# Performance work log

Hardware: AMD Instinct MI355X
Metric: run time of the kernel (lower is better)

The kernel has to match this reference:

```python
import jax, jax.numpy as jnp
import numpy as np

N = 50000   # nodes
E = 300000  # edges (before self-loops)
G = 64      # graphs in batch
F = 64      # feature_dim
H = 4       # n_head
C = 64      # per-head out channels (= feature_dim)
LAT = 256   # latent_dim
NEG_SLOPE = 0.2  # PyG GATConv default


def setup_inputs() -> dict:
    key = jax.random.key(0)
    ks = jax.random.split(key, 32)
    f32 = jnp.float32

    def w(k, shape, fan_in):
        return jax.random.normal(k, shape, dtype=f32) * (1.0 / np.sqrt(fan_in))

    return {
        "building_feature": jax.random.normal(ks[0], (N, 5), dtype=f32),
        "edge_index": jax.random.randint(ks[1], (2, E), 0, N, dtype=jnp.int32),
        "batch": jnp.sort(jax.random.randint(ks[2], (N,), 0, G, dtype=jnp.int32)),
        "bf_W": w(ks[3], (5, F), 5), "bf_b": jnp.zeros((F,), f32),
        "W1": w(ks[4], (F, H * C), F), "as1": w(ks[5], (H, C), C), "ad1": w(ks[6], (H, C), C), "b1": jnp.zeros((H * C,), f32),
        "W2": w(ks[7], (H * C, H * C), H * C), "as2": w(ks[8], (H, C), C), "ad2": w(ks[9], (H, C), C), "b2": jnp.zeros((H * C,), f32),
        "W3": w(ks[10], (H * C, H * C), H * C), "as3": w(ks[11], (H, C), C), "ad3": w(ks[12], (H, C), C), "b3": jnp.zeros((H * C,), f32),
        "agg_W": w(ks[13], (F * (1 + H * 3), LAT), F * (1 + H * 3)), "agg_b": jnp.zeros((LAT,), f32),
        "mu_W": w(ks[14], (LAT, LAT), LAT), "mu_b": jnp.zeros((LAT,), f32),
        "var_W": w(ks[15], (LAT, LAT), LAT), "var_b": jnp.zeros((LAT,), f32),
    }


def _gat_conv(x, W, att_src, att_dst, bias, src, dst):
    # PyG GATConv, concat=True, add_self_loops already in src/dst.
    h = (x @ W).reshape(-1, H, C)                       # [N,H,C]
    a_s = jnp.einsum("nhc,hc->nh", h, att_src)          # [N,H]
    a_d = jnp.einsum("nhc,hc->nh", h, att_dst)
    e = jax.nn.leaky_relu(a_s[src] + a_d[dst], NEG_SLOPE)  # [E,H]
    # segment softmax over incoming edges of each dst node
    m = jax.ops.segment_max(e, dst, num_segments=N)
    p = jnp.exp(e - m[dst])
    s = jax.ops.segment_sum(p, dst, num_segments=N)
    alpha = p / s[dst]                                  # [E,H]
    out = jax.ops.segment_sum(alpha[:, :, None] * h[src], dst, num_segments=N)
    return out.reshape(-1, H * C) + bias


def reference(building_feature, edge_index, batch,
              bf_W, bf_b,
              W1, as1, ad1, b1,
              W2, as2, ad2, b2,
              W3, as3, ad3, b3,
              agg_W, agg_b, mu_W, mu_b, var_W, var_b):
    # add self-loops (PyG GATConv default add_self_loops=True)
    loops = jnp.arange(N, dtype=edge_index.dtype)
    src = jnp.concatenate([edge_index[0], loops])
    dst = jnp.concatenate([edge_index[1], loops])

    n0 = jax.nn.relu(building_feature @ bf_W + bf_b)                 # [N,F]
    n1 = jax.nn.relu(_gat_conv(n0, W1, as1, ad1, b1, src, dst))      # [N,H*C]
    n2 = jax.nn.relu(_gat_conv(n1, W2, as2, ad2, b2, src, dst))
    n3 = jax.nn.relu(_gat_conv(n2, W3, as3, ad3, b3, src, dst))

    g = jnp.concatenate([
        jax.ops.segment_max(n0, batch, num_segments=G),
        jax.ops.segment_max(n1, batch, num_segments=G),
        jax.ops.segment_max(n2, batch, num_segments=G),
        jax.ops.segment_max(n3, batch, num_segments=G),
    ], axis=1)                                                       # [G, F*(1+3H)]

    latent = g @ agg_W + agg_b
    mu = latent @ mu_W + mu_b
    log_var = latent @ var_W + var_b
    return mu, log_var
```

## Files before the change

### kernel.cpp

```cpp
#include <hip/hip_runtime.h>
#include <hip/hip_bf16.h>

#define NN 50000
#define NPAD 50048
#define EE 300000
#define ETOT (EE + NN)
#define GG 64
#define GCOLS 832
#define LATD 256
#define BM 128
#define BN 128
#define NB_SCAN 196
#define LOG2E 1.4426950408889634f

typedef unsigned short u16;
typedef short s16x8 __attribute__((ext_vector_type(8)));
typedef float f32x4 __attribute__((ext_vector_type(4)));

__device__ __forceinline__ u16 f2bf(float f) {
    union { float f; unsigned u; } v; v.f = f;
    unsigned r = v.u + 0x7FFFu + ((v.u >> 16) & 1u);
    return (u16)(r >> 16);
}
__device__ __forceinline__ float bf2f(u16 u) {
    union { unsigned u; float f; } v; v.u = ((unsigned)u) << 16;
    return v.f;
}

__global__ __launch_bounds__(256) void k_prep(const float* __restrict__ W1, const float* __restrict__ W2,
                                              const float* __restrict__ W3, u16* __restrict__ Wt1,
                                              u16* __restrict__ Wt2, u16* __restrict__ Wt3,
                                              const float* __restrict__ bf, const float* __restrict__ Wb,
                                              const float* __restrict__ bb, const int* __restrict__ batch,
                                              u16* __restrict__ n0bf, int* __restrict__ gbuf,
                                              const int* __restrict__ ei, int* __restrict__ counts,
                                              u16* __restrict__ nbf) {
    int b = blockIdx.x;
    if (b < 576) {
        int idx = b * 256 + threadIdx.x;
        if (idx < 16384) {
            int n = idx >> 6, k = idx & 63;
            Wt1[idx] = f2bf(W1[k * 256 + n]);
        } else if (idx < 81920) {
            int t = idx - 16384; int n = t >> 8, k = t & 255;
            Wt2[t] = f2bf(W2[k * 256 + n]);
        } else {
            int t = idx - 81920; int n = t >> 8, k = t & 255;
            Wt3[t] = f2bf(W3[k * 256 + n]);
        }
    } else if (b < 967) {
        int c = threadIdx.x & 63;
        int sub = threadIdx.x >> 6;
        int base = (b - 576) * 128;
        int end = min(base + 128, NN);
        float w0 = Wb[c], w1 = Wb[64 + c], w2 = Wb[128 + c], w3 = Wb[192 + c], w4 = Wb[256 + c], bb_ = bb[c];
        float mx = 0.f;
        int curg = -1;
        for (int n = base + sub; n < end; n += 4) {
            const float* r = bf + (size_t)n * 5;
            float v = bb_ + r[0] * w0 + r[1] * w1 + r[2] * w2 + r[3] * w3 + r[4] * w4;
            v = fmaxf(v, 0.f);
            n0bf[(size_t)n * 64 + c] = f2bf(v);
            int g = batch[n];
            if (g != curg) {
                if (curg >= 0) atomicMax(&gbuf[curg * GCOLS + c], __float_as_int(mx));
                mx = 0.f; curg = g;
            }
            mx = fmaxf(mx, v);
        }
        if (curg >= 0) atomicMax(&gbuf[curg * GCOLS + c], __float_as_int(mx));
    } else if (b < 2335) {
        int e = (b - 967) * 256 + threadIdx.x;
        if (e < ETOT) {
            int d = (e < EE) ? ei[EE + e] : (e - EE);
            atomicAdd(&counts[d], 1);
        }
    } else {
        u16* p0 = n0bf + (size_t)NN * 64;
        for (int i = threadIdx.x; i < (NPAD - NN) * 64; i += 256) p0[i] = 0;
        u16* p1 = nbf + (size_t)NN * 256;
        for (int i = threadIdx.x; i < (NPAD - NN) * 256; i += 256) p1[i] = 0;
    }
}

__global__ __launch_bounds__(256) void k_scan_block(const int* __restrict__ counts, int* __restrict__ scanned,
                                                    int* __restrict__ bsums, int n) {
    __shared__ int sh[256];
    int i = blockIdx.x * 256 + threadIdx.x;
    int v = (i < n) ? counts[i] : 0;
    sh[threadIdx.x] = v; __syncthreads();
    for (int d = 1; d < 256; d <<= 1) {
        int t = (threadIdx.x >= d) ? sh[threadIdx.x - d] : 0;
        __syncthreads();
        sh[threadIdx.x] += t;
        __syncthreads();
    }
    if (i < n) scanned[i] = sh[threadIdx.x] - v;
    if (threadIdx.x == 255) bsums[blockIdx.x] = sh[255];
}

__global__ __launch_bounds__(256) void k_scan_add2(const int* __restrict__ scanned, const int* __restrict__ bsums,
                                                   int* __restrict__ indptr, int* __restrict__ fill) {
    __shared__ int sh[256];
    int t = threadIdx.x;
    int v = (t < NB_SCAN) ? bsums[t] : 0;
    sh[t] = v; __syncthreads();
    for (int d = 1; d < 256; d <<= 1) {
        int u = (t >= d) ? sh[t - d] : 0;
        __syncthreads();
        sh[t] += u;
        __syncthreads();
    }
    int bix = blockIdx.x;
    int boff = (bix == 0) ? 0 : sh[bix - 1];
    int i = bix * 256 + t;
    if (i < NN) { indptr[i] = scanned[i] + boff; fill[i] = 0; }
    if (i == 0) indptr[NN] = ETOT;
}

__global__ __launch_bounds__(256) void k_fill(const int* __restrict__ ei, const int* __restrict__ indptr,
                                              int* __restrict__ fill, int* __restrict__ esrc) {
    int e = blockIdx.x * 256 + threadIdx.x;
    if (e >= ETOT) return;
    int s, d;
    if (e < EE) { s = ei[e]; d = ei[EE + e]; } else { s = d = e - EE; }
    int pos = atomicAdd(&fill[d], 1);
    esrc[indptr[d] + pos] = s;
}

__global__ __launch_bounds__(256) void k_gemm_mfma(const u16* __restrict__ A,
                                                   const u16* __restrict__ Bt,
                                                   const float* __restrict__ att_s,
                                                   const float* __restrict__ att_d,
                                                   u16* __restrict__ Hbf,
                                                   float* __restrict__ a_s,
                                                   float* __restrict__ a_d,
                                                   int K) {
    __shared__ __align__(16) u16 As[128 * 64];
    __shared__ __align__(16) u16 Bs[128 * 64];
    const int tid = threadIdx.x;
    const int lane = tid & 63;
    const int w = tid >> 6;
    const int wr = w >> 1, wc = w & 1;
    const int row0 = blockIdx.x * BM;
    const int col0 = blockIdx.y * BN;

    f32x4 acc[4][4] = {};

    for (int kt = 0; kt < K; kt += 64) {
#pragma unroll
        for (int i = 0; i < 4; ++i) {
            int u = i * 256 + tid;
            int r = u >> 3, c16 = u & 7;
            int sc = ((c16 ^ (r & 7)) << 3);
            const u16* ga = A + (size_t)(row0 + r) * K + kt + sc;
            u16* la = &As[(size_t)(i * 256 + (w << 6)) * 8];
            __builtin_amdgcn_global_load_lds((const __attribute__((address_space(1))) void*)ga,
                                             (__attribute__((address_space(3))) void*)la, 16, 0, 0);
        }
#pragma unroll
        for (int i = 0; i < 4; ++i) {
            int u = i * 256 + tid;
            int r = u >> 3, c16 = u & 7;
            int sc = ((c16 ^ (r & 7)) << 3);
            const u16* gb = Bt + (size_t)(col0 + r) * K + kt + sc;
            u16* lb = &Bs[(size_t)(i * 256 + (w << 6)) * 8];
            __builtin_amdgcn_global_load_lds((const __attribute__((address_space(1))) void*)gb,
                                             (__attribute__((address_space(3))) void*)lb, 16, 0, 0);
        }
        __syncthreads();
#pragma unroll
        for (int ks = 0; ks < 2; ++ks) {
            s16x8 af[4], bfr[4];
#pragma unroll
            for (int m = 0; m < 4; ++m) {
                int ra = wr * 64 + m * 16 + (lane & 15);
                int c16 = ks * 4 + (lane >> 4);
                int off = ra * 64 + ((c16 ^ (ra & 7)) << 3);
                af[m] = *reinterpret_cast<const s16x8*>(&As[off]);
            }
#pragma unroll
            for (int n = 0; n < 4; ++n) {
                int rb = wc * 64 + n * 16 + (lane & 15);
                int c16 = ks * 4 + (lane >> 4);
                int off = rb * 64 + ((c16 ^ (rb & 7)) << 3);
                bfr[n] = *reinterpret_cast<const s16x8*>(&Bs[off]);
            }
#pragma unroll
            for (int m = 0; m < 4; ++m)
#pragma unroll
                for (int n = 0; n < 4; ++n)
                    acc[m][n] = __builtin_amdgcn_mfma_f32_16x16x32_bf16(af[m], bfr[n], acc[m][n], 0, 0, 0);
        }
        __syncthreads();
    }

    const int head = (blockIdx.y << 1) + wc;
    float asv[4], adv[4];
#pragma unroll
    for (int n = 0; n < 4; ++n) {
        asv[n] = att_s[head * 64 + n * 16 + (lane & 15)] * LOG2E;
        adv[n] = att_d[head * 64 + n * 16 + (lane & 15)] * LOG2E;
    }
#pragma unroll
    for (int m = 0; m < 4; ++m) {
        int growb = row0 + wr * 64 + m * 16 + (lane >> 4) * 4;
#pragma unroll
        for (int j = 0; j < 4; ++j) {
            int grow = growb + j;
            u16* orow = Hbf + (size_t)grow * 256 + col0 + wc * 64 + (lane & 15);
            float vs = 0.f, vd = 0.f;
#pragma unroll
            for (int n = 0; n < 4; ++n) {
                float v = acc[m][n][j];
                orow[n * 16] = f2bf(v);
                vs += v * asv[n];
                vd += v * adv[n];
            }
            vs += __shfl_xor(vs, 1); vd += __shfl_xor(vd, 1);
            vs += __shfl_xor(vs, 2); vd += __shfl_xor(vd, 2);
            vs += __shfl_xor(vs, 4); vd += __shfl_xor(vd, 4);
            vs += __shfl_xor(vs, 8); vd += __shfl_xor(vd, 8);
            if ((lane & 15) == 0) {
                a_s[grow * 4 + head] = vs;
                a_d[grow * 4 + head] = vd;
            }
        }
    }
}

__global__ __launch_bounds__(1024) void k_agg(const u16* __restrict__ Hbf, const float* __restrict__ a_s,
                                              const float* __restrict__ a_d, const int* __restrict__ indptr,
                                              const int* __restrict__ esrc, const float* __restrict__ bias,
                                              const int* __restrict__ batch, u16* __restrict__ outbf,
                                              int* __restrict__ gbuf, int poolOff) {
    __shared__ int lpool[2][256];
    if (threadIdx.x < 512) lpool[threadIdx.x >> 8][threadIdx.x & 255] = 0;
    __syncthreads();

    const int nodeBase = blockIdx.x * 16;
    const int wv = threadIdx.x >> 6;
    const int wid = nodeBase + wv;
    const int lane = threadIdx.x & 63;
    const int h = lane >> 4;
    const int eidx = lane & 15;
    const bool active = wid < NN;

    if (active) {
        int beg = indptr[wid];
        int dcount = indptr[wid + 1] - beg;
        float ad = a_d[wid * 4 + h];
        float mx = -3.0e38f, ssum = 0.f;
        float ax = 0.f, ay = 0.f, az = 0.f, aw = 0.f;

        for (int cb = 0; cb < dcount; cb += 16) {
            int cnt = min(16, dcount - cb);
            int s = (eidx < cnt) ? esrc[beg + cb + eidx] : 0;
            float el = (eidx < cnt) ? a_s[s * 4 + h] + ad : -3.0e38f;
            el = fmaxf(el, 0.2f * el);
            float cm = el;
            cm = fmaxf(cm, __shfl_xor(cm, 1));
            cm = fmaxf(cm, __shfl_xor(cm, 2));
            cm = fmaxf(cm, __shfl_xor(cm, 4));
            cm = fmaxf(cm, __shfl_xor(cm, 8));
            float nm = fmaxf(mx, cm);
            if (__any(nm > mx)) {
                float corr = exp2f(mx - nm);
                ssum *= corr; ax *= corr; ay *= corr; az *= corr; aw *= corr;
                mx = nm;
            }
            float p = exp2f(el - mx);
            float cs = p;
            cs += __shfl_xor(cs, 1);
            cs += __shfl_xor(cs, 2);
            cs += __shfl_xor(cs, 4);
            cs += __shfl_xor(cs, 8);
            ssum += cs;
            int e2 = 0;
            for (; e2 + 2 <= cnt; e2 += 2) {
                int s0 = __shfl(s, e2), s1 = __shfl(s, e2 + 1);
                float p0 = __shfl(p, (lane & 48) | e2);
                float p1 = __shfl(p, (lane & 48) | (e2 + 1));
                const ushort4 h0 = *reinterpret_cast<const ushort4*>(Hbf + (size_t)s0 * 256 + lane * 4);
                const ushort4 h1 = *reinterpret_cast<const ushort4*>(Hbf + (size_t)s1 * 256 + lane * 4);
                ax += p0 * bf2f(h0.x) + p1 * bf2f(h1.x);
                ay += p0 * bf2f(h0.y) + p1 * bf2f(h1.y);
                az += p0 * bf2f(h0.z) + p1 * bf2f(h1.z);
                aw += p0 * bf2f(h0.w) + p1 * bf2f(h1.w);
            }
            if (e2 < cnt) {
                int s0 = __shfl(s, e2);
                float p0 = __shfl(p, (lane & 48) | e2);
                const ushort4 h0 = *reinterpret_cast<const ushort4*>(Hbf + (size_t)s0 * 256 + lane * 4);
                ax += p0 * bf2f(h0.x);
                ay += p0 * bf2f(h0.y);
                az += p0 * bf2f(h0.z);
                aw += p0 * bf2f(h0.w);
            }
        }

        float inv = 1.0f / ssum;
        const float4 bv = *reinterpret_cast<const float4*>(bias + lane * 4);
        float o0 = fmaxf(ax * inv + bv.x, 0.f);
        float o1 = fmaxf(ay * inv + bv.y, 0.f);
        float o2 = fmaxf(az * inv + bv.z, 0.f);
        float o3 = fmaxf(aw * inv + bv.w, 0.f);
        ushort4 ob; ob.x = f2bf(o0); ob.y = f2bf(o1); ob.z = f2bf(o2); ob.w = f2bf(o3);
        *reinterpret_cast<ushort4*>(outbf + (size_t)wid * 256 + lane * 4) = ob;

        int g = batch[wid];
        int g0 = batch[nodeBase];
        int slot = g - g0;
        int c4 = lane * 4;
        if (slot < 2) {
            atomicMax(&lpool[slot][c4],     __float_as_int(o0));
            atomicMax(&lpool[slot][c4 + 1], __float_as_int(o1));
            atomicMax(&lpool[slot][c4 + 2], __float_as_int(o2));
            atomicMax(&lpool[slot][c4 + 3], __float_as_int(o3));
        } else {
            int* cell = &gbuf[g * GCOLS + poolOff + c4];
            atomicMax(cell,     __float_as_int(o0));
            atomicMax(cell + 1, __float_as_int(o1));
            atomicMax(cell + 2, __float_as_int(o2));
            atomicMax(cell + 3, __float_as_int(o3));
        }
    }
    __syncthreads();
    if (threadIdx.x < 512) {
        int slot = threadIdx.x >> 8, c = threadIdx.x & 255;
        int v = lpool[slot][c];
        if (v != 0) {
            int g0 = batch[nodeBase];
            atomicMax(&gbuf[(g0 + slot) * GCOLS + poolOff + c], v);
        }
    }
}

__global__ __launch_bounds__(256) void k_head(const int* __restrict__ gbuf,
                                              const float* __restrict__ aggW, const float* __restrict__ aggb,
                                              const float* __restrict__ muW, const float* __restrict__ mub,
                                              const float* __restrict__ varW, const float* __restrict__ varb,
                                              float* __restrict__ out) {
    __shared__ float lat[LATD];
    int gi = blockIdx.x, j = threadIdx.x;
    const float* g = (const float*)gbuf + (size_t)gi * GCOLS;
    float acc = aggb[j];
    for (int k = 0; k < GCOLS; ++k) acc += g[k] * aggW[k * 256 + j];
    lat[j] = acc;
    __syncthreads();
    float am = mub[j], av = varb[j];
    for (int k = 0; k < 256; ++k) {
        float l = lat[k];
        am += l * muW[k * 256 + j];
        av += l * varW[k * 256 + j];
    }
    out[(size_t)gi * 256 + j] = am;
    out[(size_t)GG * 256 + (size_t)gi * 256 + j] = av;
}

extern "C" void kernel_launch(void* const* d_in, const int* in_sizes, int n_in,
                              void* d_out, int out_size, void* d_ws, size_t ws_size,
                              hipStream_t stream) {
    const float* bf   = (const float*)d_in[0];
    const int*   ei   = (const int*)d_in[1];
    const int*   batch= (const int*)d_in[2];
    const float* bf_W = (const float*)d_in[3];
    const float* bf_b = (const float*)d_in[4];
    const float* W1   = (const float*)d_in[5];
    const float* as1  = (const float*)d_in[6];
    const float* ad1  = (const float*)d_in[7];
    const float* b1   = (const float*)d_in[8];
    const float* W2   = (const float*)d_in[9];
    const float* as2  = (const float*)d_in[10];
    const float* ad2  = (const float*)d_in[11];
    const float* b2   = (const float*)d_in[12];
    const float* W3   = (const float*)d_in[13];
    const float* as3  = (const float*)d_in[14];
    const float* ad3  = (const float*)d_in[15];
    const float* b3   = (const float*)d_in[16];
    const float* aggW = (const float*)d_in[17];
    const float* aggb = (const float*)d_in[18];
    const float* muW  = (const float*)d_in[19];
    const float* mub  = (const float*)d_in[20];
    const float* varW = (const float*)d_in[21];
    const float* varb = (const float*)d_in[22];
    float* out = (float*)d_out;

    size_t off = 0;
    auto alloc = [&](size_t bytes) -> char* {
        char* p = (char*)d_ws + off;
        off += (bytes + 255) & ~(size_t)255;
        return p;
    };
    int*   counts  = (int*)alloc((size_t)(NN + GG * GCOLS) * 4);
    int*   gbuf    = counts + NN;
    u16*   Hbf     = (u16*)alloc((size_t)NPAD * 256 * 2);
    u16*   n0bf    = (u16*)alloc((size_t)NPAD * 64 * 2);
    u16*   nbf     = (u16*)alloc((size_t)NPAD * 256 * 2);
    float* a_s     = (float*)alloc((size_t)NPAD * 4 * 4);
    float* a_d     = (float*)alloc((size_t)NPAD * 4 * 4);
    int*   scanned = (int*)alloc((size_t)NN * 4);
    int*   bsums   = (int*)alloc(256 * 4);
    int*   indptr  = (int*)alloc((size_t)(NN + 1) * 4);
    int*   fill    = (int*)alloc((size_t)NN * 4);
    int*   esrc    = (int*)alloc((size_t)ETOT * 4);
    u16*   Wt1     = (u16*)alloc((size_t)256 * 64 * 2);
    u16*   Wt2     = (u16*)alloc((size_t)256 * 256 * 2);
    u16*   Wt3     = (u16*)alloc((size_t)256 * 256 * 2);

    hipMemsetAsync(counts, 0, (size_t)(NN + GG * GCOLS) * 4, stream);

    k_prep<<<2336, 256, 0, stream>>>(W1, W2, W3, Wt1, Wt2, Wt3,
                                     bf, bf_W, bf_b, batch, n0bf, gbuf,
                                     ei, counts, nbf);

    k_scan_block<<<NB_SCAN, 256, 0, stream>>>(counts, scanned, bsums, NN);
    k_scan_add2<<<NB_SCAN, 256, 0, stream>>>(scanned, bsums, indptr, fill);
    k_fill<<<(ETOT + 255) / 256, 256, 0, stream>>>(ei, indptr, fill, esrc);

    dim3 ggrid(NPAD / BM, 256 / BN);
    const int AB = NN / 16;

    k_gemm_mfma<<<ggrid, 256, 0, stream>>>(n0bf, Wt1, as1, ad1, Hbf, a_s, a_d, 64);
    k_agg<<<AB, 1024, 0, stream>>>(Hbf, a_s, a_d, indptr, esrc, b1, batch, nbf, gbuf, 64);

    k_gemm_mfma<<<ggrid, 256, 0, stream>>>(nbf, Wt2, as2, ad2, Hbf, a_s, a_d, 256);
    k_agg<<<AB, 1024, 0, stream>>>(Hbf, a_s, a_d, indptr, esrc, b2, batch, nbf, gbuf, 320);

    k_gemm_mfma<<<ggrid, 256, 0, stream>>>(nbf, Wt3, as3, ad3, Hbf, a_s, a_d, 256);
    k_agg<<<AB, 1024, 0, stream>>>(Hbf, a_s, a_d, indptr, esrc, b3, batch, nbf, gbuf, 576);

    k_head<<<GG, 256, 0, stream>>>(gbuf, aggW, aggb, muW, mub, varW, varb, out);
}
```

Measured before the change: 275.9 us.

## Shrink aggregation blocks, unroll gather by four, restructure pooling and split head GEMV

The aggregation kernel now uses 8-node, 512-thread blocks with no bounds check, since 50000 divides evenly by 8. Its gather loop is unrolled to four edges per step so more loads are in flight. Per-block graph max-pooling now goes through a shared-memory reduction instead of shared atomics. The head kernel spreads each GEMV's K dimension across 1024 threads and reduces the partials in shared memory, which addresses the low parallelism of 64 blocks of 256 threads. The trade-offs are more aggregation blocks and more register pressure from the unroll.

```diff
diff --git a/kernel.cpp b/kernel.cpp
--- a/kernel.cpp
+++ b/kernel.cpp
@@ -229,133 +229,134 @@
     }
 }
 
-__global__ __launch_bounds__(1024) void k_agg(const u16* __restrict__ Hbf, const float* __restrict__ a_s,
-                                              const float* __restrict__ a_d, const int* __restrict__ indptr,
-                                              const int* __restrict__ esrc, const float* __restrict__ bias,
-                                              const int* __restrict__ batch, u16* __restrict__ outbf,
-                                              int* __restrict__ gbuf, int poolOff) {
-    __shared__ int lpool[2][256];
-    if (threadIdx.x < 512) lpool[threadIdx.x >> 8][threadIdx.x & 255] = 0;
-    __syncthreads();
-
-    const int nodeBase = blockIdx.x * 16;
+__global__ __launch_bounds__(512) void k_agg(const u16* __restrict__ Hbf, const float* __restrict__ a_s,
+                                             const float* __restrict__ a_d, const int* __restrict__ indptr,
+                                             const int* __restrict__ esrc, const float* __restrict__ bias,
+                                             const int* __restrict__ batch, u16* __restrict__ outbf,
+                                             int* __restrict__ gbuf, int poolOff) {
+    __shared__ float smax[8][256];
+    __shared__ int sb[8];
+    const int nodeBase = blockIdx.x * 8;
     const int wv = threadIdx.x >> 6;
     const int wid = nodeBase + wv;
     const int lane = threadIdx.x & 63;
     const int h = lane >> 4;
     const int eidx = lane & 15;
-    const bool active = wid < NN;
-
-    if (active) {
-        int beg = indptr[wid];
-        int dcount = indptr[wid + 1] - beg;
-        float ad = a_d[wid * 4 + h];
-        float mx = -3.0e38f, ssum = 0.f;
-        float ax = 0.f, ay = 0.f, az = 0.f, aw = 0.f;
-
-        for (int cb = 0; cb < dcount; cb += 16) {
-            int cnt = min(16, dcount - cb);
-            int s = (eidx < cnt) ? esrc[beg + cb + eidx] : 0;
-            float el = (eidx < cnt) ? a_s[s * 4 + h] + ad : -3.0e38f;
-            el = fmaxf(el, 0.2f * el);
-            float cm = el;
-            cm = fmaxf(cm, __shfl_xor(cm, 1));
-            cm = fmaxf(cm, __shfl_xor(cm, 2));
-            cm = fmaxf(cm, __shfl_xor(cm, 4));
-            cm = fmaxf(cm, __shfl_xor(cm, 8));
-            float nm = fmaxf(mx, cm);
-            if (__any(nm > mx)) {
-                float corr = exp2f(mx - nm);
-                ssum *= corr; ax *= corr; ay *= corr; az *= corr; aw *= corr;
-                mx = nm;
-            }
-            float p = exp2f(el - mx);
-            float cs = p;
-            cs += __shfl_xor(cs, 1);
-            cs += __shfl_xor(cs, 2);
-            cs += __shfl_xor(cs, 4);
-            cs += __shfl_xor(cs, 8);
-            ssum += cs;
-            int e2 = 0;
-            for (; e2 + 2 <= cnt; e2 += 2) {
-                int s0 = __shfl(s, e2), s1 = __shfl(s, e2 + 1);
-                float p0 = __shfl(p, (lane & 48) | e2);
-                float p1 = __shfl(p, (lane & 48) | (e2 + 1));
-                const ushort4 h0 = *reinterpret_cast<const ushort4*>(Hbf + (size_t)s0 * 256 + lane * 4);
-                const ushort4 h1 = *reinterpret_cast<const ushort4*>(Hbf + (size_t)s1 * 256 + lane * 4);
-                ax += p0 * bf2f(h0.x) + p1 * bf2f(h1.x);
-                ay += p0 * bf2f(h0.y) + p1 * bf2f(h1.y);
-                az += p0 * bf2f(h0.z) + p1 * bf2f(h1.z);
-                aw += p0 * bf2f(h0.w) + p1 * bf2f(h1.w);
-            }
-            if (e2 < cnt) {
-                int s0 = __shfl(s, e2);
-                float p0 = __shfl(p, (lane & 48) | e2);
-                const ushort4 h0 = *reinterpret_cast<const ushort4*>(Hbf + (size_t)s0 * 256 + lane * 4);
-                ax += p0 * bf2f(h0.x);
-                ay += p0 * bf2f(h0.y);
-                az += p0 * bf2f(h0.z);
-                aw += p0 * bf2f(h0.w);
-            }
-        }
-
-        float inv = 1.0f / ssum;
-        const float4 bv = *reinterpret_cast<const float4*>(bias + lane * 4);
-        float o0 = fmaxf(ax * inv + bv.x, 0.f);
-        float o1 = fmaxf(ay * inv + bv.y, 0.f);
-        float o2 = fmaxf(az * inv + bv.z, 0.f);
-        float o3 = fmaxf(aw * inv + bv.w, 0.f);
-        ushort4 ob; ob.x = f2bf(o0); ob.y = f2bf(o1); ob.z = f2bf(o2); ob.w = f2bf(o3);
-        *reinterpret_cast<ushort4*>(outbf + (size_t)wid * 256 + lane * 4) = ob;
-
-        int g = batch[wid];
-        int g0 = batch[nodeBase];
-        int slot = g - g0;
-        int c4 = lane * 4;
-        if (slot < 2) {
-            atomicMax(&lpool[slot][c4],     __float_as_int(o0));
-            atomicMax(&lpool[slot][c4 + 1], __float_as_int(o1));
-            atomicMax(&lpool[slot][c4 + 2], __float_as_int(o2));
-            atomicMax(&lpool[slot][c4 + 3], __float_as_int(o3));
-        } else {
-            int* cell = &gbuf[g * GCOLS + poolOff + c4];
-            atomicMax(cell,     __float_as_int(o0));
-            atomicMax(cell + 1, __float_as_int(o1));
-            atomicMax(cell + 2, __float_as_int(o2));
-            atomicMax(cell + 3, __float_as_int(o3));
-        }
-    }
+
+    if (threadIdx.x < 8) sb[threadIdx.x] = batch[nodeBase + threadIdx.x];
     __syncthreads();
-    if (threadIdx.x < 512) {
-        int slot = threadIdx.x >> 8, c = threadIdx.x & 255;
-        int v = lpool[slot][c];
-        if (v != 0) {
-            int g0 = batch[nodeBase];
-            atomicMax(&gbuf[(g0 + slot) * GCOLS + poolOff + c], v);
-        }
-    }
-}
-
-__global__ __launch_bounds__(256) void k_head(const int* __restrict__ gbuf,
-                                              const float* __restrict__ aggW, const float* __restrict__ aggb,
-                                              const float* __restrict__ muW, const float* __restrict__ mub,
-                                              const float* __restrict__ varW, const float* __restrict__ varb,
-                                              float* __restrict__ out) {
+
+    int beg = indptr[wid];
+    int dcount = indptr[wid + 1] - beg;
+    float ad = a_d[wid * 4 + h];
+    float mx = -3.0e38f, ssum = 0.f;
+    float ax = 0.f, ay = 0.f, az = 0.f, aw = 0.f;
+
+    for (int cb = 0; cb < dcount; cb += 16) {
+        int cnt = min(16, dcount - cb);
+        int s = (eidx < cnt) ? esrc[beg + cb + eidx] : 0;
+        float el = (eidx < cnt) ? a_s[s * 4 + h] + ad : -3.0e38f;
+        el = fmaxf(el, 0.2f * el);
+        float cm = el;
+        cm = fmaxf(cm, __shfl_xor(cm, 1));
+        cm = fmaxf(cm, __shfl_xor(cm, 2));
+        cm = fmaxf(cm, __shfl_xor(cm, 4));
+        cm = fmaxf(cm, __shfl_xor(cm, 8));
+        float nm = fmaxf(mx, cm);
+        if (__any(nm > mx)) {
+            float corr = exp2f(mx - nm);
+            ssum *= corr; ax *= corr; ay *= corr; az *= corr; aw *= corr;
+            mx = nm;
+        }
+        float p = exp2f(el - mx);
+        float cs = p;
+        cs += __shfl_xor(cs, 1);
+        cs += __shfl_xor(cs, 2);
+        cs += __shfl_xor(cs, 4);
+        cs += __shfl_xor(cs, 8);
+        ssum += cs;
+        int e2 = 0;
+        for (; e2 + 4 <= cnt; e2 += 4) {
+            int s0 = __shfl(s, e2), s1 = __shfl(s, e2 + 1), s2 = __shfl(s, e2 + 2), s3 = __shfl(s, e2 + 3);
+            float p0 = __shfl(p, (lane & 48) | e2);
+            float p1 = __shfl(p, (lane & 48) | (e2 + 1));
+            float p2 = __shfl(p, (lane & 48) | (e2 + 2));
+            float p3 = __shfl(p, (lane & 48) | (e2 + 3));
+            const ushort4 h0 = *reinterpret_cast<const ushort4*>(Hbf + (size_t)s0 * 256 + lane * 4);
+            const ushort4 h1 = *reinterpret_cast<const ushort4*>(Hbf + (size_t)s1 * 256 + lane * 4);
+            const ushort4 h2 = *reinterpret_cast<const ushort4*>(Hbf + (size_t)s2 * 256 + lane * 4);
+            const ushort4 h3 = *reinterpret_cast<const ushort4*>(Hbf + (size_t)s3 * 256 + lane * 4);
+            ax += p0 * bf2f(h0.x) + p1 * bf2f(h1.x) + p2 * bf2f(h2.x) + p3 * bf2f(h3.x);
+            ay += p0 * bf2f(h0.y) + p1 * bf2f(h1.y) + p2 * bf2f(h2.y) + p3 * bf2f(h3.y);
+            az += p0 * bf2f(h0.z) + p1 * bf2f(h1.z) + p2 * bf2f(h2.z) + p3 * bf2f(h3.z);
+            aw += p0 * bf2f(h0.w) + p1 * bf2f(h1.w) + p2 * bf2f(h2.w) + p3 * bf2f(h3.w);
+        }
+        for (; e2 < cnt; ++e2) {
+            int s0 = __shfl(s, e2);
+            float p0 = __shfl(p, (lane & 48) | e2);
+            const ushort4 h0 = *reinterpret_cast<const ushort4*>(Hbf + (size_t)s0 * 256 + lane * 4);
+            ax += p0 * bf2f(h0.x);
+            ay += p0 * bf2f(h0.y);
+            az += p0 * bf2f(h0.z);
+            aw += p0 * bf2f(h0.w);
+        }
+    }
+
+    float inv = 1.0f / ssum;
+    const float4 bv = *reinterpret_cast<const float4*>(bias + lane * 4);
+    float o0 = fmaxf(ax * inv + bv.x, 0.f);
+    float o1 = fmaxf(ay * inv + bv.y, 0.f);
+    float o2 = fmaxf(az * inv + bv.z, 0.f);
+    float o3 = fmaxf(aw * inv + bv.w, 0.f);
+    ushort4 ob; ob.x = f2bf(o0); ob.y = f2bf(o1); ob.z = f2bf(o2); ob.w = f2bf(o3);
+    *reinterpret_cast<ushort4*>(outbf + (size_t)wid * 256 + lane * 4) = ob;
+
+    *reinterpret_cast<float4*>(&smax[wv][lane * 4]) = make_float4(o0, o1, o2, o3);
+    int slot = sb[wv] - sb[0];
+    if (slot >= 2) {
+        int* cell = &gbuf[sb[wv] * GCOLS + poolOff + lane * 4];
+        atomicMax(cell,     __float_as_int(o0));
+        atomicMax(cell + 1, __float_as_int(o1));
+        atomicMax(cell + 2, __float_as_int(o2));
+        atomicMax(cell + 3, __float_as_int(o3));
+    }
+    __syncthreads();
+
+    int slotf = threadIdx.x >> 8;
+    int c = threadIdx.x & 255;
+    int gtar = sb[0] + slotf;
+    float m = 0.f;
+#pragma unroll
+    for (int n = 0; n < 8; ++n)
+        if (sb[n] == gtar) m = fmaxf(m, smax[n][c]);
+    if (m > 0.f) atomicMax(&gbuf[gtar * GCOLS + poolOff + c], __float_as_int(m));
+}
+
+__global__ __launch_bounds__(1024) void k_head(const int* __restrict__ gbuf,
+                                               const float* __restrict__ aggW, const float* __restrict__ aggb,
+                                               const float* __restrict__ muW, const float* __restrict__ mub,
+                                               const float* __restrict__ varW, const float* __restrict__ varb,
+                                               float* __restrict__ out) {
+    __shared__ float part[4][256];
     __shared__ float lat[LATD];
-    int gi = blockIdx.x, j = threadIdx.x;
+    int gi = blockIdx.x;
+    int j = threadIdx.x & 255, ks = threadIdx.x >> 8;
     const float* g = (const float*)gbuf + (size_t)gi * GCOLS;
-    float acc = aggb[j];
-    for (int k = 0; k < GCOLS; ++k) acc += g[k] * aggW[k * 256 + j];
-    lat[j] = acc;
+    float acc = 0.f;
+    int k0 = ks * 208;
+    for (int k = k0; k < k0 + 208; ++k) acc += g[k] * aggW[k * 256 + j];
+    part[ks][j] = acc;
     __syncthreads();
-    float am = mub[j], av = varb[j];
-    for (int k = 0; k < 256; ++k) {
-        float l = lat[k];
-        am += l * muW[k * 256 + j];
-        av += l * varW[k * 256 + j];
-    }
-    out[(size_t)gi * 256 + j] = am;
-    out[(size_t)GG * 256 + (size_t)gi * 256 + j] = av;
+    if (ks == 0) lat[j] = part[0][j] + part[1][j] + part[2][j] + part[3][j] + aggb[j];
+    __syncthreads();
+    const float* W = (ks < 2) ? muW : varW;
+    int kb = (ks & 1) * 128;
+    float am = 0.f;
+    for (int k = kb; k < kb + 128; ++k) am += lat[k] * W[k * 256 + j];
+    part[ks][j] = am;
+    __syncthreads();
+    if (ks == 0) out[(size_t)gi * 256 + j] = part[0][j] + part[1][j] + mub[j];
+    else if (ks == 1) out[(size_t)GG * 256 + (size_t)gi * 256 + j] = part[2][j] + part[3][j] + varb[j];
 }
 
 extern "C" void kernel_launch(void* const* d_in, const int* in_sizes, int n_in,
@@ -419,16 +420,16 @@
     k_fill<<<(ETOT + 255) / 256, 256, 0, stream>>>(ei, indptr, fill, esrc);
 
     dim3 ggrid(NPAD / BM, 256 / BN);
-    const int AB = NN / 16;
+    const int AB = NN / 8;
 
     k_gemm_mfma<<<ggrid, 256, 0, stream>>>(n0bf, Wt1, as1, ad1, Hbf, a_s, a_d, 64);
-    k_agg<<<AB, 1024, 0, stream>>>(Hbf, a_s, a_d, indptr, esrc, b1, batch, nbf, gbuf, 64);
+    k_agg<<<AB, 512, 0, stream>>>(Hbf, a_s, a_d, indptr, esrc, b1, batch, nbf, gbuf, 64);
 
     k_gemm_mfma<<<ggrid, 256, 0, stream>>>(nbf, Wt2, as2, ad2, Hbf, a_s, a_d, 256);
-    k_agg<<<AB, 1024, 0, stream>>>(Hbf, a_s, a_d, indptr, esrc, b2, batch, nbf, gbuf, 320);
+    k_agg<<<AB, 512, 0, stream>>>(Hbf, a_s, a_d, indptr, esrc, b2, batch, nbf, gbuf, 320);
 
     k_gemm_mfma<<<ggrid, 256, 0, stream>>>(nbf, Wt3, as3, ad3, Hbf, a_s, a_d, 256);
-    k_agg<<<AB, 1024, 0, stream>>>(Hbf, a_s, a_d, indptr, esrc, b3, batch, nbf, gbuf, 576);
-
-    k_head<<<GG, 256, 0, stream>>>(gbuf, aggW, aggb, muW, mub, varW, varb, out);
-}
+    k_agg<<<AB, 512, 0, stream>>>(Hbf, a_s, a_d, indptr, esrc, b3, batch, nbf, gbuf, 576);
+
+    k_head<<<GG, 1024, 0, stream>>>(gbuf, aggW, aggb, muW, mub, varW, varb, out);
+}
```

Result: no change. 273.8 us (-0.8%).
